# Optimization experiments

Hardware: AMD Instinct MI355X
Metric: run time of the kernel (lower is better)

Reference implementation:

```python
import jax, jax.numpy as jnp
import numpy as np

B, L, E, A, H = 1024, 200, 128, 128, 4

def setup_inputs() -> dict:
    key = jax.random.key(0)
    k1, k2, k3, k4, k5, k6 = jax.random.split(key, 6)
    inp = jax.random.normal(k1, (B, L, E), dtype=jnp.float32)
    mask = jax.random.randint(k2, (B, L), 0, 2).astype(bool)
    # guarantee at least one valid position per row (realistic: histories are non-empty)
    mask = mask.at[:, 0].set(True)
    pos_enc = jax.random.normal(k3, (1, L, E), dtype=jnp.float32)
    W1 = jax.random.normal(k4, (E, A), dtype=jnp.float32) / np.sqrt(E)
    W2 = jax.random.normal(k5, (A, H), dtype=jnp.float32) / np.sqrt(A)
    W_out = jax.random.normal(k6, (H * E, E), dtype=jnp.float32) / np.sqrt(H * E)
    return {"input": inp, "mask": mask, "pos_enc": pos_enc, "W1": W1, "W2": W2, "W_out": W_out}

def reference(input, mask, pos_enc, W1, W2, W_out):
    fm = mask.astype(input.dtype)[..., None]          # [B, L, 1]
    x = input * fm                                     # zero out padded positions
    xp = x + pos_enc                                   # broadcast [1, L, E]
    hidden = jnp.tanh(xp @ W1)                         # [B, L, A]
    att = hidden @ W2                                  # [B, L, H]
    att = jnp.swapaxes(att, 1, 2)                      # [B, H, L]
    neg = jnp.asarray(-(2.0 ** 32) + 1.0, dtype=att.dtype)
    att = jnp.where(mask[:, None, :], att, neg)
    att = jax.nn.softmax(att, axis=-1)                 # [B, H, L]
    pooled = jnp.einsum('bhl,ble->bhe', att, x)        # [B, H, E]
    flat = pooled.reshape(pooled.shape[0], -1)         # [B, H*E]
    return flat @ W_out                                # [B, E]
```

## Files before the change

kernel.cpp:

```cpp
#include <hip/hip_runtime.h>
#include <cfloat>

#define Bn 1024
#define Ln 200
#define En 128
#define An 128
#define Hn 4

#define WS_POSW1   0
#define WS_W1FRAG  106496
#define WS_ATTPOOL 139264
#define SLOT       1664
#define WS_WOUTT   1843200
#define WS_NEEDED  1974272

using f32x4  = __attribute__((ext_vector_type(4))) float;
using bf16x8 = __attribute__((ext_vector_type(8))) short;

__device__ __forceinline__ unsigned short f2bf(float f){
    unsigned u = __builtin_bit_cast(unsigned, f);
    u = (u + 0x7FFFu + ((u >> 16) & 1u)) >> 16;
    return (unsigned short)u;
}
__device__ __forceinline__ float bf2f(unsigned short s){
    unsigned u = ((unsigned)s) << 16;
    return __builtin_bit_cast(float, u);
}
__device__ __forceinline__ unsigned short f2h(float f){
    _Float16 h = (_Float16)f;
    return __builtin_bit_cast(unsigned short, h);
}
__device__ __forceinline__ float h2f(unsigned short s){
    _Float16 h = __builtin_bit_cast(_Float16, s);
    return (float)h;
}
__device__ __forceinline__ float tanh_cheap(float x){
    float e = __expf(2.f * x);
    float r = __builtin_amdgcn_rcpf(e + 1.f);
    return fmaf(-2.f, r, 1.f);
}
__device__ __forceinline__ float tanh_fast(float x){
    x = fminf(fmaxf(x, -12.f), 12.f);
    float e = __expf(2.f * x);
    return 1.f - 2.f / (e + 1.f);
}
__device__ __forceinline__ unsigned cvt_pk_bf16(float lo, float hi){
    unsigned r;
    asm("v_cvt_pk_bf16_f32 %0, %1, %2" : "=v"(r) : "v"(lo), "v"(hi));
    return r;
}
__device__ __forceinline__ int swz(int row, int k){
    return row * 128 + ((((k >> 3) ^ (row & 15)) << 3) | (k & 7));
}

__global__ __launch_bounds__(256) void sap_prep(
    const float* __restrict__ pos, const float* __restrict__ W1,
    const float* __restrict__ Wout, void* __restrict__ ws)
{
    const int t = threadIdx.x, blk = blockIdx.x;
    if (blk < 104){
        float* posW1 = (float*)((char*)ws + WS_POSW1);
        int l = blk * 2 + (t >> 7), a = t & 127;
        float acc = 0.f;
        if (l < Ln){
            #pragma unroll 4
            for (int k = 0; k < 128; ++k)
                acc += pos[l * En + k] * W1[k * An + a];
        }
        posW1[l * An + a] = acc;
    } else if (blk < 106){
        unsigned short* w1f = (unsigned short*)((char*)ws + WS_W1FRAG);
        int s = (blk - 104) * 256 + t;
        int lane = s & 63, A = s >> 6;
        int c = lane & 15, q = lane >> 4;
        #pragma unroll
        for (int ks = 0; ks < 4; ++ks){
            unsigned short v[8];
            #pragma unroll
            for (int j = 0; j < 8; ++j)
                v[j] = f2bf(W1[(ks * 32 + q * 8 + j) * An + A * 16 + c]);
            *(bf16x8*)&w1f[((s) * 4 + ks) * 8] = *(bf16x8*)v;
        }
    } else {
        unsigned short* wt = (unsigned short*)((char*)ws + WS_WOUTT);
        int flat = ((blk - 106) * 256 + t) * 4;
        int e = flat >> 9, k = flat & 511;
        unsigned short v[4];
        #pragma unroll
        for (int i = 0; i < 4; ++i)
            v[i] = f2bf(Wout[(size_t)(k + i) * En + e]);
        *(uint2*)&wt[flat] = *(uint2*)v;
    }
}

__global__ __launch_bounds__(512, 6) void sap_att5(
    const float* __restrict__ inp, const void* __restrict__ maskp,
    const float* __restrict__ W2, void* __restrict__ ws)
{
    __shared__ unsigned short s_x[64 * 128];
    __shared__ float s_part[8][4][64];
    __shared__ float s_mask[64];

    const int t = threadIdx.x, lane = t & 63, w = t >> 6;
    const int c = lane & 15, q = lane >> 4;
    const int b = blockIdx.x, chunk = blockIdx.y;
    const int l0 = chunk * 64;
    const int NT = (chunk < 3) ? 4 : 1;
    const int nv = (chunk < 3) ? 64 : (Ln - 192);

    const unsigned short* w1f   = (const unsigned short*)((char*)ws + WS_W1FRAG);
    const float*          posW1 = (const float*)((char*)ws + WS_POSW1);
    unsigned short*       slot  = (unsigned short*)((char*)ws + WS_ATTPOOL + (size_t)b * SLOT);

    {
        unsigned word = ((const unsigned*)maskp)[lane];
        unsigned long long bi = __ballot(word > 1u);
        unsigned long long bf = __ballot(word != 0u && word != 0x3F800000u);
        const int flag = (bi == 0ull) ? 0 : ((bf == 0ull) ? 2 : 1);
        if (t < 64){
            float m = 0.f;
            int l = l0 + t;
            if (l < Ln){
                int mv;
                if (flag == 0)      mv = ((const int*)maskp)[b * Ln + l] != 0;
                else if (flag == 1) mv = ((const unsigned char*)maskp)[b * Ln + l] != 0;
                else                mv = ((const float*)maskp)[b * Ln + l] != 0.f;
                m = mv ? 1.f : 0.f;
            }
            s_mask[t] = m;
        }
    }

    {
        const float4* in4 = (const float4*)(inp + ((size_t)b * Ln + l0) * En);
        if (chunk < 3){
            float4 u0 = in4[t], u1 = in4[t + 512], u2 = in4[t + 1024], u3 = in4[t + 1536];
            #define PUTV(vi, idx) { int ll = (idx) >> 5, kk = ((idx) & 31) * 4;               \
                uint2 val = make_uint2(cvt_pk_bf16(vi.x, vi.y), cvt_pk_bf16(vi.z, vi.w));     \
                *(uint2*)&s_x[swz(ll, kk)] = val; }
            PUTV(u0, t) PUTV(u1, t + 512) PUTV(u2, t + 1024) PUTV(u3, t + 1536)
            #undef PUTV
        } else {
            uint2 val = make_uint2(0u, 0u);
            if (t < 256){
                float4 u0 = in4[t];
                val = make_uint2(cvt_pk_bf16(u0.x, u0.y), cvt_pk_bf16(u0.z, u0.w));
            }
            int ll = t >> 5, kk = (t & 31) * 4;
            *(uint2*)&s_x[swz(ll, kk)] = val;
        }
    }

    bf16x8 af[4];
    #pragma unroll
    for (int ks = 0; ks < 4; ++ks)
        af[ks] = *(const bf16x8*)&w1f[((w * 64 + lane) * 4 + ks) * 8];
    float4 w2a[4];
    #pragma unroll
    for (int v = 0; v < 4; ++v)
        w2a[v] = *(const float4*)&W2[(w * 16 + q * 4 + v) * Hn];

    __syncthreads();

    for (int lt = 0; lt < NT; ++lt){
        int brow = lt * 16 + c;
        bf16x8 bfr[4];
        #pragma unroll
        for (int ks = 0; ks < 4; ++ks){
            int g = (ks * 4 + q) ^ c;
            bfr[ks] = *(bf16x8*)&s_x[brow * 128 + (g << 3)];
        }
        f32x4 acc = *(const f32x4*)&posW1[(size_t)(l0 + lt * 16 + c) * An + w * 16 + q * 4];
        #pragma unroll
        for (int ks = 0; ks < 4; ++ks)
            acc = __builtin_amdgcn_mfma_f32_16x16x32_bf16(af[ks], bfr[ks], acc, 0, 0, 0);
        float contrib[4] = {0.f, 0.f, 0.f, 0.f};
        #pragma unroll
        for (int v = 0; v < 4; ++v){
            float hv = tanh_cheap(acc[v]);
            contrib[0] += hv * w2a[v].x;
            contrib[1] += hv * w2a[v].y;
            contrib[2] += hv * w2a[v].z;
            contrib[3] += hv * w2a[v].w;
        }
        #pragma unroll
        for (int h = 0; h < 4; ++h){
            contrib[h] += __shfl_xor(contrib[h], 16, 64);
            contrib[h] += __shfl_xor(contrib[h], 32, 64);
        }
        s_part[w][q][lt * 16 + c] = contrib[q];
    }
    __syncthreads();

    if (t < 256){
        int h = t >> 6, ll = t & 63;
        if (ll < nv){
            float s = 0.f;
            #pragma unroll
            for (int w2 = 0; w2 < 8; ++w2) s += s_part[w2][h][ll];
            float v = (s_mask[ll] > 0.5f) ? s : -65504.f;
            slot[h * Ln + l0 + ll] = f2h(v);
        }
    }
}

__global__ __launch_bounds__(256, 8) void sap_pool(
    const float* __restrict__ inp, void* __restrict__ ws)
{
    __shared__ float s_att4[Ln * 4];
    __shared__ float s_scr[8][512];

    const int t = threadIdx.x, lane = t & 63, w = t >> 6;
    const int b = blockIdx.x;
    unsigned short* slot = (unsigned short*)((char*)ws + WS_ATTPOOL + (size_t)b * SLOT);

    {
        const int h = w;
        float v[4]; float mx = -FLT_MAX;
        #pragma unroll
        for (int i = 0; i < 4; ++i){
            int l = lane + i * 64;
            v[i] = (l < Ln) ? h2f(slot[h * Ln + l]) : -65504.f;
            mx = fmaxf(mx, v[i]);
        }
        for (int s = 32; s; s >>= 1) mx = fmaxf(mx, __shfl_xor(mx, s, 64));
        float e[4]; float sum = 0.f;
        #pragma unroll
        for (int i = 0; i < 4; ++i){
            int l = lane + i * 64;
            e[i] = (l < Ln) ? __expf(v[i] - mx) : 0.f;
            sum += e[i];
        }
        for (int s = 32; s; s >>= 1) sum += __shfl_xor(sum, s, 64);
        float inv = 1.f / sum;
        #pragma unroll
        for (int i = 0; i < 4; ++i){
            int l = lane + i * 64;
            if (l < Ln) s_att4[l * 4 + h] = e[i] * inv;
        }
    }
    __syncthreads();

    {
        const int eg = t & 31, r = t >> 5;
        const float* xin = inp + (size_t)b * (Ln * En);
        f32x4 acc0 = {0.f,0.f,0.f,0.f}, acc1 = acc0, acc2 = acc0, acc3 = acc0;
        for (int i = 0; i < 25; ++i){
            int l = i * 8 + r;
            f32x4 xv = *(const f32x4*)&xin[l * En + eg * 4];
            f32x4 a4 = *(const f32x4*)&s_att4[l * 4];
            acc0 += xv * a4[0];
            acc1 += xv * a4[1];
            acc2 += xv * a4[2];
            acc3 += xv * a4[3];
        }
        *(f32x4*)&s_scr[r][0 * 128 + eg * 4] = acc0;
        *(f32x4*)&s_scr[r][1 * 128 + eg * 4] = acc1;
        *(f32x4*)&s_scr[r][2 * 128 + eg * 4] = acc2;
        *(f32x4*)&s_scr[r][3 * 128 + eg * 4] = acc3;
    }
    __syncthreads();

    for (int s2 = t; s2 < 512; s2 += 256){
        float sum = 0.f;
        #pragma unroll
        for (int r2 = 0; r2 < 8; ++r2) sum += s_scr[r2][s2];
        slot[s2] = f2bf(sum);
    }
}

__global__ __launch_bounds__(256) void sap_out(
    const void* __restrict__ ws, float* __restrict__ out)
{
    const unsigned short* wt = (const unsigned short*)((const char*)ws + WS_WOUTT);
    const int t = threadIdx.x, lane = t & 63, w = t >> 6;
    const int c = lane & 15, q = lane >> 4;
    const int b0 = blockIdx.x * 16;
    const int e0 = (blockIdx.y * 4 + w) * 16;

    const unsigned short* pslot =
        (const unsigned short*)((const char*)ws + WS_ATTPOOL + (size_t)(b0 + c) * SLOT);

    f32x4 acc = {0.f, 0.f, 0.f, 0.f};
    #pragma unroll 4
    for (int ks = 0; ks < 16; ++ks){
        bf16x8 afr = *(const bf16x8*)&pslot[ks * 32 + q * 8];
        bf16x8 bfr = *(const bf16x8*)&wt[(e0 + c) * 512 + ks * 32 + q * 8];
        acc = __builtin_amdgcn_mfma_f32_16x16x32_bf16(afr, bfr, acc, 0, 0, 0);
    }
    #pragma unroll
    for (int v = 0; v < 4; ++v)
        out[(size_t)(b0 + q * 4 + v) * En + e0 + c] = acc[v];
}

__global__ __launch_bounds__(512, 4) void sap_fused_v2(
    const float* __restrict__ inp, const void* __restrict__ maskp,
    const float* __restrict__ pos, const float* __restrict__ W1,
    const float* __restrict__ W2, const float* __restrict__ Wout,
    float* __restrict__ out)
{
#define LP 208
    __shared__ unsigned short s_xp [LP * 128];
    __shared__ float s_att [4 * LP];
    __shared__ float s_mask[LP];
    __shared__ float s_pool[512];
    __shared__ float s_red [512];
    __shared__ int   s_flag;

    const int t = threadIdx.x;
    const int b = blockIdx.x;
    const int lane = t & 63, w = t >> 6;
    const int c = lane & 15, q = lane >> 4;

    if (t == 0){
        const unsigned* mw = (const unsigned*)maskp;
        int fi = 1, ff = 1;
        for (int i = 0; i < 64; ++i){
            unsigned word = mw[i];
            if (word > 1u) fi = 0;
            if (word != 0u && word != 0x3F800000u) ff = 0;
        }
        s_flag = fi ? 0 : (ff ? 2 : 1);
    }
    bf16x8 af[4];
    {
        const int arow = w * 16 + c;
        #pragma unroll
        for (int ks = 0; ks < 4; ++ks)
            #pragma unroll
            for (int j = 0; j < 8; ++j)
                af[ks][j] = (short)f2bf(W1[(ks * 32 + q * 8 + j) * An + arow]);
    }
    float w2a[4][4];
    #pragma unroll
    for (int v = 0; v < 4; ++v){
        float4 wv = *(const float4*)&W2[(w * 16 + q * 4 + v) * Hn];
        w2a[v][0] = wv.x; w2a[v][1] = wv.y; w2a[v][2] = wv.z; w2a[v][3] = wv.w;
    }
    __syncthreads();
    const int flag = s_flag;
    for (int l = t; l < LP; l += 512){
        float m = 0.f;
        if (l < Ln){
            int mv;
            if (flag == 0)      mv = ((const int*)maskp)[b * Ln + l] != 0;
            else if (flag == 1) mv = ((const unsigned char*)maskp)[b * Ln + l] != 0;
            else                mv = ((const float*)maskp)[b * Ln + l] != 0.f;
            m = mv ? 1.f : 0.f;
        }
        s_mask[l] = m;
    }
    for (int i = t; i < 4 * LP; i += 512) s_att[i] = 0.f;
    __syncthreads();
    {
        const float4* in4 = (const float4*)(inp + (size_t)b * (Ln * En));
        const float4* p4  = (const float4*)pos;
        #pragma unroll
        for (int it = 0; it < 13; ++it){
            int idx = it * 512 + t;
            int l = idx >> 5;
            int k = (idx & 31) * 4;
            uint2 val;
            if (idx < 6400){
                float m = s_mask[l];
                float4 a = in4[idx];
                float4 p = p4[idx];
                val = make_uint2((unsigned)f2bf(a.x*m+p.x) | ((unsigned)f2bf(a.y*m+p.y) << 16),
                                 (unsigned)f2bf(a.z*m+p.z) | ((unsigned)f2bf(a.w*m+p.w) << 16));
            } else val = make_uint2(0u, 0u);
            *(uint2*)&s_xp[swz(l, k)] = val;
        }
    }
    __syncthreads();
    for (int lt = 0; lt < 13; ++lt){
        int brow = lt * 16 + c;
        bf16x8 bfr[4];
        #pragma unroll
        for (int ks = 0; ks < 4; ++ks){
            int g = (ks * 4 + q) ^ c;
            bfr[ks] = *(bf16x8*)&s_xp[brow * 128 + (g << 3)];
        }
        f32x4 acc = {0.f, 0.f, 0.f, 0.f};
        #pragma unroll
        for (int ks = 0; ks < 4; ++ks)
            acc = __builtin_amdgcn_mfma_f32_16x16x32_bf16(af[ks], bfr[ks], acc, 0, 0, 0);
        float hv[4];
        #pragma unroll
        for (int v = 0; v < 4; ++v) hv[v] = tanh_fast(acc[v]);
        #pragma unroll
        for (int h = 0; h < 4; ++h){
            float contrib = hv[0]*w2a[0][h] + hv[1]*w2a[1][h] + hv[2]*w2a[2][h] + hv[3]*w2a[3][h];
            contrib += __shfl_xor(contrib, 16, 64);
            contrib += __shfl_xor(contrib, 32, 64);
            if (lane < 16) atomicAdd(&s_att[h * LP + lt * 16 + lane], contrib);
        }
    }
    __syncthreads();
    if (t < 256){
        const int sl = t & 63, h = t >> 6;
        float v[4]; bool ok[4]; float mx = -FLT_MAX;
        #pragma unroll
        for (int i = 0; i < 4; ++i){
            int l = sl + i * 64;
            ok[i] = (l < Ln) && (s_mask[l] > 0.5f);
            v[i]  = ok[i] ? s_att[h * LP + l] : -FLT_MAX;
            mx = fmaxf(mx, v[i]);
        }
        for (int s = 32; s; s >>= 1) mx = fmaxf(mx, __shfl_xor(mx, s, 64));
        float e[4]; float sum = 0.f;
        #pragma unroll
        for (int i = 0; i < 4; ++i){ e[i] = ok[i] ? __expf(v[i]-mx) : 0.f; sum += e[i]; }
        for (int s = 32; s; s >>= 1) sum += __shfl_xor(sum, s, 64);
        float inv = 1.f / sum;
        #pragma unroll
        for (int i = 0; i < 4; ++i){ int l = sl + i*64; if (l < LP) s_att[h*LP+l] = e[i]*inv; }
    }
    __syncthreads();
    {
        int h = t >> 7, e = t & 127;
        float acc = 0.f;
        #pragma unroll 4
        for (int l = 0; l < Ln; ++l){
            float xv = bf2f(s_xp[swz(l, e)]) - pos[l * En + e];
            acc += s_att[h * LP + l] * xv;
        }
        s_pool[h * En + e] = acc;
    }
    __syncthreads();
    {
        int qt = t >> 7, e = t & 127;
        float acc = 0.f;
        const float* wo = Wout + (size_t)(qt * 128) * En + e;
        #pragma unroll 4
        for (int i = 0; i < 128; ++i)
            acc += s_pool[qt * 128 + i] * wo[(size_t)i * En];
        s_red[t] = acc;
    }
    __syncthreads();
    if (t < 128)
        out[(size_t)b * En + t] = s_red[t] + s_red[t + 128] + s_red[t + 256] + s_red[t + 384];
#undef LP
}

extern "C" void kernel_launch(void* const* d_in, const int* in_sizes, int n_in,
                              void* d_out, int out_size, void* d_ws, size_t ws_size,
                              hipStream_t stream)
{
    const float* inp  = (const float*)d_in[0];
    const void*  mask = d_in[1];
    const float* pos  = (const float*)d_in[2];
    const float* W1   = (const float*)d_in[3];
    const float* W2   = (const float*)d_in[4];
    const float* Wout = (const float*)d_in[5];
    float* out = (float*)d_out;

    if (ws_size >= WS_NEEDED){
        sap_prep<<<170, 256, 0, stream>>>(pos, W1, Wout, d_ws);
        sap_att5<<<dim3(Bn, 4), 512, 0, stream>>>(inp, mask, W2, d_ws);
        sap_pool<<<Bn, 256, 0, stream>>>(inp, d_ws);
        sap_out<<<dim3(64, 2), 256, 0, stream>>>(d_ws, out);
    } else {
        sap_fused_v2<<<Bn, 512, 0, stream>>>(inp, mask, pos, W1, W2, Wout, out);
    }
}
```

Measured before the change: 70.63 us.

## Fuse attention scoring and pooling into one kernel with online softmax

Merges the per-chunk attention-score kernel and the softmax/pooling kernel into a single per-batch kernel. It walks the 200 positions in four 64-row chunks with a double-buffered bf16 LDS tile and keeps a running max and sum for softmax. Pooling reads the bf16 tile already staged in LDS, so the second global read of the input is gone, along with the fp16 score round-trip through the workspace and one launch. In exchange each block now has 4x less grid parallelism, runs serial chunk loops with extra barriers, and pools from bf16-rounded inputs instead of fp32.

Result: slower. 95.37 us (+35.0%).

```diff
diff --git a/kernel.cpp b/kernel.cpp
--- a/kernel.cpp
+++ b/kernel.cpp
@@ -25,14 +25,6 @@
 __device__ __forceinline__ float bf2f(unsigned short s){
     unsigned u = ((unsigned)s) << 16;
     return __builtin_bit_cast(float, u);
-}
-__device__ __forceinline__ unsigned short f2h(float f){
-    _Float16 h = (_Float16)f;
-    return __builtin_bit_cast(unsigned short, h);
-}
-__device__ __forceinline__ float h2f(unsigned short s){
-    _Float16 h = __builtin_bit_cast(_Float16, s);
-    return (float)h;
 }
 __device__ __forceinline__ float tanh_cheap(float x){
     float e = __expf(2.f * x);
@@ -71,7 +63,8 @@
     } else if (blk < 106){
         unsigned short* w1f = (unsigned short*)((char*)ws + WS_W1FRAG);
         int s = (blk - 104) * 256 + t;
-        int lane = s & 63, A = s >> 6;
+        int lane = s & 63;
+        int A = s >> 6;
         int c = lane & 15, q = lane >> 4;
         #pragma unroll
         for (int ks = 0; ks < 4; ++ks){
@@ -79,7 +72,7 @@
             #pragma unroll
             for (int j = 0; j < 8; ++j)
                 v[j] = f2bf(W1[(ks * 32 + q * 8 + j) * An + A * 16 + c]);
-            *(bf16x8*)&w1f[((s) * 4 + ks) * 8] = *(bf16x8*)v;
+            *(bf16x8*)&w1f[(s * 4 + ks) * 8] = *(bf16x8*)v;
         }
     } else {
         unsigned short* wt = (unsigned short*)((char*)ws + WS_WOUTT);
@@ -93,63 +86,24 @@
     }
 }
 
-__global__ __launch_bounds__(512, 6) void sap_att5(
+__global__ __launch_bounds__(512, 6) void sap_main3(
     const float* __restrict__ inp, const void* __restrict__ maskp,
     const float* __restrict__ W2, void* __restrict__ ws)
 {
-    __shared__ unsigned short s_x[64 * 128];
+    __shared__ unsigned short s_x[2][64 * 128];
     __shared__ float s_part[8][4][64];
-    __shared__ float s_mask[64];
+    __shared__ float s_w[4][64];
+    __shared__ float s_scale[4];
+    __shared__ float s_zfin[4];
 
     const int t = threadIdx.x, lane = t & 63, w = t >> 6;
     const int c = lane & 15, q = lane >> 4;
-    const int b = blockIdx.x, chunk = blockIdx.y;
-    const int l0 = chunk * 64;
-    const int NT = (chunk < 3) ? 4 : 1;
-    const int nv = (chunk < 3) ? 64 : (Ln - 192);
+    const int b = blockIdx.x;
+    const int hh = t >> 7, ee = t & 127;
 
     const unsigned short* w1f   = (const unsigned short*)((char*)ws + WS_W1FRAG);
     const float*          posW1 = (const float*)((char*)ws + WS_POSW1);
     unsigned short*       slot  = (unsigned short*)((char*)ws + WS_ATTPOOL + (size_t)b * SLOT);
-
-    {
-        unsigned word = ((const unsigned*)maskp)[lane];
-        unsigned long long bi = __ballot(word > 1u);
-        unsigned long long bf = __ballot(word != 0u && word != 0x3F800000u);
-        const int flag = (bi == 0ull) ? 0 : ((bf == 0ull) ? 2 : 1);
-        if (t < 64){
-            float m = 0.f;
-            int l = l0 + t;
-            if (l < Ln){
-                int mv;
-                if (flag == 0)      mv = ((const int*)maskp)[b * Ln + l] != 0;
-                else if (flag == 1) mv = ((const unsigned char*)maskp)[b * Ln + l] != 0;
-                else                mv = ((const float*)maskp)[b * Ln + l] != 0.f;
-                m = mv ? 1.f : 0.f;
-            }
-            s_mask[t] = m;
-        }
-    }
-
-    {
-        const float4* in4 = (const float4*)(inp + ((size_t)b * Ln + l0) * En);
-        if (chunk < 3){
-            float4 u0 = in4[t], u1 = in4[t + 512], u2 = in4[t + 1024], u3 = in4[t + 1536];
-            #define PUTV(vi, idx) { int ll = (idx) >> 5, kk = ((idx) & 31) * 4;               \
-                uint2 val = make_uint2(cvt_pk_bf16(vi.x, vi.y), cvt_pk_bf16(vi.z, vi.w));     \
-                *(uint2*)&s_x[swz(ll, kk)] = val; }
-            PUTV(u0, t) PUTV(u1, t + 512) PUTV(u2, t + 1024) PUTV(u3, t + 1536)
-            #undef PUTV
-        } else {
-            uint2 val = make_uint2(0u, 0u);
-            if (t < 256){
-                float4 u0 = in4[t];
-                val = make_uint2(cvt_pk_bf16(u0.x, u0.y), cvt_pk_bf16(u0.z, u0.w));
-            }
-            int ll = t >> 5, kk = (t & 31) * 4;
-            *(uint2*)&s_x[swz(ll, kk)] = val;
-        }
-    }
 
     bf16x8 af[4];
     #pragma unroll
@@ -160,113 +114,122 @@
     for (int v = 0; v < 4; ++v)
         w2a[v] = *(const float4*)&W2[(w * 16 + q * 4 + v) * Hn];
 
-    __syncthreads();
-
-    for (int lt = 0; lt < NT; ++lt){
-        int brow = lt * 16 + c;
-        bf16x8 bfr[4];
-        #pragma unroll
-        for (int ks = 0; ks < 4; ++ks){
-            int g = (ks * 4 + q) ^ c;
-            bfr[ks] = *(bf16x8*)&s_x[brow * 128 + (g << 3)];
-        }
-        f32x4 acc = *(const f32x4*)&posW1[(size_t)(l0 + lt * 16 + c) * An + w * 16 + q * 4];
-        #pragma unroll
-        for (int ks = 0; ks < 4; ++ks)
-            acc = __builtin_amdgcn_mfma_f32_16x16x32_bf16(af[ks], bfr[ks], acc, 0, 0, 0);
-        float contrib[4] = {0.f, 0.f, 0.f, 0.f};
-        #pragma unroll
-        for (int v = 0; v < 4; ++v){
-            float hv = tanh_cheap(acc[v]);
-            contrib[0] += hv * w2a[v].x;
-            contrib[1] += hv * w2a[v].y;
-            contrib[2] += hv * w2a[v].z;
-            contrib[3] += hv * w2a[v].w;
-        }
-        #pragma unroll
-        for (int h = 0; h < 4; ++h){
-            contrib[h] += __shfl_xor(contrib[h], 16, 64);
-            contrib[h] += __shfl_xor(contrib[h], 32, 64);
-        }
-        s_part[w][q][lt * 16 + c] = contrib[q];
-    }
-    __syncthreads();
-
-    if (t < 256){
-        int h = t >> 6, ll = t & 63;
-        if (ll < nv){
-            float s = 0.f;
-            #pragma unroll
-            for (int w2 = 0; w2 < 8; ++w2) s += s_part[w2][h][ll];
-            float v = (s_mask[ll] > 0.5f) ? s : -65504.f;
-            slot[h * Ln + l0 + ll] = f2h(v);
-        }
-    }
-}
-
-__global__ __launch_bounds__(256, 8) void sap_pool(
-    const float* __restrict__ inp, void* __restrict__ ws)
-{
-    __shared__ float s_att4[Ln * 4];
-    __shared__ float s_scr[8][512];
-
-    const int t = threadIdx.x, lane = t & 63, w = t >> 6;
-    const int b = blockIdx.x;
-    unsigned short* slot = (unsigned short*)((char*)ws + WS_ATTPOOL + (size_t)b * SLOT);
-
-    {
-        const int h = w;
-        float v[4]; float mx = -FLT_MAX;
-        #pragma unroll
-        for (int i = 0; i < 4; ++i){
-            int l = lane + i * 64;
-            v[i] = (l < Ln) ? h2f(slot[h * Ln + l]) : -65504.f;
-            mx = fmaxf(mx, v[i]);
-        }
-        for (int s = 32; s; s >>= 1) mx = fmaxf(mx, __shfl_xor(mx, s, 64));
-        float e[4]; float sum = 0.f;
-        #pragma unroll
-        for (int i = 0; i < 4; ++i){
-            int l = lane + i * 64;
-            e[i] = (l < Ln) ? __expf(v[i] - mx) : 0.f;
-            sum += e[i];
-        }
-        for (int s = 32; s; s >>= 1) sum += __shfl_xor(sum, s, 64);
-        float inv = 1.f / sum;
-        #pragma unroll
-        for (int i = 0; i < 4; ++i){
-            int l = lane + i * 64;
-            if (l < Ln) s_att4[l * 4 + h] = e[i] * inv;
-        }
-    }
-    __syncthreads();
-
-    {
-        const int eg = t & 31, r = t >> 5;
-        const float* xin = inp + (size_t)b * (Ln * En);
-        f32x4 acc0 = {0.f,0.f,0.f,0.f}, acc1 = acc0, acc2 = acc0, acc3 = acc0;
-        for (int i = 0; i < 25; ++i){
-            int l = i * 8 + r;
-            f32x4 xv = *(const f32x4*)&xin[l * En + eg * 4];
-            f32x4 a4 = *(const f32x4*)&s_att4[l * 4];
-            acc0 += xv * a4[0];
-            acc1 += xv * a4[1];
-            acc2 += xv * a4[2];
-            acc3 += xv * a4[3];
-        }
-        *(f32x4*)&s_scr[r][0 * 128 + eg * 4] = acc0;
-        *(f32x4*)&s_scr[r][1 * 128 + eg * 4] = acc1;
-        *(f32x4*)&s_scr[r][2 * 128 + eg * 4] = acc2;
-        *(f32x4*)&s_scr[r][3 * 128 + eg * 4] = acc3;
-    }
-    __syncthreads();
-
-    for (int s2 = t; s2 < 512; s2 += 256){
-        float sum = 0.f;
-        #pragma unroll
-        for (int r2 = 0; r2 < 8; ++r2) sum += s_scr[r2][s2];
-        slot[s2] = f2bf(sum);
-    }
+    int flag;
+    {
+        unsigned word = ((const unsigned*)maskp)[lane];
+        unsigned long long bi = __ballot(word > 1u);
+        unsigned long long bfm = __ballot(word != 0u && word != 0x3F800000u);
+        flag = (bi == 0ull) ? 0 : ((bfm == 0ull) ? 2 : 1);
+    }
+
+    const float4* in4 = (const float4*)(inp + (size_t)b * (Ln * En));
+
+    {
+        float4 u0 = in4[t], u1 = in4[t + 512], u2 = in4[t + 1024], u3 = in4[t + 1536];
+        #define PUTV(buf, vi, idx) { int ll = (idx) >> 5, kk = ((idx) & 31) * 4;             \
+            uint2 val = make_uint2(cvt_pk_bf16(vi.x, vi.y), cvt_pk_bf16(vi.z, vi.w));        \
+            *(uint2*)&s_x[buf][swz(ll, kk)] = val; }
+        PUTV(0, u0, t) PUTV(0, u1, t + 512) PUTV(0, u2, t + 1024) PUTV(0, u3, t + 1536)
+    }
+    __syncthreads();
+
+    float accp = 0.f;
+    float Mh = -3.0e38f, Zh = 0.f;
+
+    for (int cch = 0; cch < 4; ++cch){
+        const int cur = cch & 1;
+        const int NT = (cch < 3) ? 4 : 1;
+
+        for (int lt = 0; lt < NT; ++lt){
+            int brow = lt * 16 + c;
+            bf16x8 bfr[4];
+            #pragma unroll
+            for (int ks = 0; ks < 4; ++ks){
+                int g = (ks * 4 + q) ^ c;
+                bfr[ks] = *(bf16x8*)&s_x[cur][brow * 128 + (g << 3)];
+            }
+            f32x4 acc = *(const f32x4*)&posW1[(size_t)(cch * 64 + lt * 16 + c) * An + w * 16 + q * 4];
+            #pragma unroll
+            for (int ks = 0; ks < 4; ++ks)
+                acc = __builtin_amdgcn_mfma_f32_16x16x32_bf16(af[ks], bfr[ks], acc, 0, 0, 0);
+            float contrib[4] = {0.f, 0.f, 0.f, 0.f};
+            #pragma unroll
+            for (int v = 0; v < 4; ++v){
+                float hv = tanh_cheap(acc[v]);
+                contrib[0] += hv * w2a[v].x;
+                contrib[1] += hv * w2a[v].y;
+                contrib[2] += hv * w2a[v].z;
+                contrib[3] += hv * w2a[v].w;
+            }
+            #pragma unroll
+            for (int h = 0; h < 4; ++h){
+                contrib[h] += __shfl_xor(contrib[h], 16, 64);
+                contrib[h] += __shfl_xor(contrib[h], 32, 64);
+            }
+            s_part[w][q][lt * 16 + c] = contrib[q];
+        }
+        __syncthreads();
+
+        float4 u0, u1, u2, u3;
+        if (cch < 3){
+            const int base = (cch + 1) * 2048;
+            const float4 z4 = make_float4(0.f, 0.f, 0.f, 0.f);
+            u0 = (base + t        < 6400) ? in4[base + t]        : z4;
+            u1 = (base + t + 512  < 6400) ? in4[base + t + 512]  : z4;
+            u2 = (base + t + 1024 < 6400) ? in4[base + t + 1024] : z4;
+            u3 = (base + t + 1536 < 6400) ? in4[base + t + 1536] : z4;
+        }
+
+        if (t < 256){
+            const int h = t >> 6, l = t & 63;
+            float att = 0.f;
+            #pragma unroll
+            for (int w2 = 0; w2 < 8; ++w2) att += s_part[w2][h][l];
+            int gl = cch * 64 + l;
+            int mv = 0;
+            if (gl < Ln){
+                if (flag == 0)      mv = ((const int*)maskp)[b * Ln + gl] != 0;
+                else if (flag == 1) mv = ((const unsigned char*)maskp)[b * Ln + gl] != 0;
+                else                mv = ((const float*)maskp)[b * Ln + gl] != 0.f;
+            }
+            att = mv ? att : -1.0e30f;
+            float cm = att;
+            #pragma unroll
+            for (int s = 32; s; s >>= 1) cm = fmaxf(cm, __shfl_xor(cm, s, 64));
+            float Mn = fmaxf(Mh, cm);
+            float sc = __expf(Mh - Mn);
+            float wl = __expf(att - Mn);
+            float zc = wl;
+            #pragma unroll
+            for (int s = 32; s; s >>= 1) zc += __shfl_xor(zc, s, 64);
+            Zh = Zh * sc + zc;
+            Mh = Mn;
+            s_w[h][l] = wl;
+            if (l == 0){
+                s_scale[h] = sc;
+                if (cch == 3) s_zfin[h] = Zh;
+            }
+        }
+        __syncthreads();
+
+        {
+            float a = accp * s_scale[hh];
+            #pragma unroll 8
+            for (int l = 0; l < 64; ++l)
+                a = fmaf(s_w[hh][l], bf2f(s_x[cur][swz(l, ee)]), a);
+            accp = a;
+        }
+
+        if (cch < 3){
+            const int base = (cch + 1) * 2048, nxt = cur ^ 1;
+            (void)base;
+            PUTV(nxt, u0, t) PUTV(nxt, u1, t + 512) PUTV(nxt, u2, t + 1024) PUTV(nxt, u3, t + 1536)
+        }
+        __syncthreads();
+    }
+    #undef PUTV
+
+    slot[hh * En + ee] = f2bf(accp * (1.f / s_zfin[hh]));
 }
 
 __global__ __launch_bounds__(256) void sap_out(
@@ -456,8 +419,7 @@
 
     if (ws_size >= WS_NEEDED){
         sap_prep<<<170, 256, 0, stream>>>(pos, W1, Wout, d_ws);
-        sap_att5<<<dim3(Bn, 4), 512, 0, stream>>>(inp, mask, W2, d_ws);
-        sap_pool<<<Bn, 256, 0, stream>>>(inp, d_ws);
+        sap_main3<<<Bn, 512, 0, stream>>>(inp, mask, W2, d_ws);
         sap_out<<<dim3(64, 2), 256, 0, stream>>>(d_ws, out);
     } else {
         sap_fused_v2<<<Bn, 512, 0, stream>>>(inp, mask, pos, W1, W2, Wout, out);
```

## Fuse attention-score and pooling kernels into one per-batch block

Applied to the files above, without the earlier changes.

Merges the per-chunk attention-score kernel and the softmax/pooling kernel into a single kernel with one 512-thread block per batch row. The block loops over the four 64-position chunks, keeps the scores in shared memory in fp32, and then runs the softmax and weighted pooling in place. This removes one kernel launch and the fp16 score round trip through global workspace. In exchange the grid drops from 4096 to 1024 blocks, shared memory per block grows, and the chunk loop runs serially with two barriers per chunk, which may reduce parallelism and latency hiding.

Result: faster. 64.60 us (-8.5%).

```diff
diff --git a/kernel.cpp b/kernel.cpp
--- a/kernel.cpp
+++ b/kernel.cpp
@@ -25,14 +25,6 @@
 __device__ __forceinline__ float bf2f(unsigned short s){
     unsigned u = ((unsigned)s) << 16;
     return __builtin_bit_cast(float, u);
-}
-__device__ __forceinline__ unsigned short f2h(float f){
-    _Float16 h = (_Float16)f;
-    return __builtin_bit_cast(unsigned short, h);
-}
-__device__ __forceinline__ float h2f(unsigned short s){
-    _Float16 h = __builtin_bit_cast(_Float16, s);
-    return (float)h;
 }
 __device__ __forceinline__ float tanh_cheap(float x){
     float e = __expf(2.f * x);
@@ -71,7 +63,8 @@
     } else if (blk < 106){
         unsigned short* w1f = (unsigned short*)((char*)ws + WS_W1FRAG);
         int s = (blk - 104) * 256 + t;
-        int lane = s & 63, A = s >> 6;
+        int lane = s & 63;
+        int A = s >> 6;
         int c = lane & 15, q = lane >> 4;
         #pragma unroll
         for (int ks = 0; ks < 4; ++ks){
@@ -79,7 +72,7 @@
             #pragma unroll
             for (int j = 0; j < 8; ++j)
                 v[j] = f2bf(W1[(ks * 32 + q * 8 + j) * An + A * 16 + c]);
-            *(bf16x8*)&w1f[((s) * 4 + ks) * 8] = *(bf16x8*)v;
+            *(bf16x8*)&w1f[(s * 4 + ks) * 8] = *(bf16x8*)v;
         }
     } else {
         unsigned short* wt = (unsigned short*)((char*)ws + WS_WOUTT);
@@ -93,63 +86,23 @@
     }
 }
 
-__global__ __launch_bounds__(512, 6) void sap_att5(
+__global__ __launch_bounds__(512, 4) void sap_att7(
     const float* __restrict__ inp, const void* __restrict__ maskp,
     const float* __restrict__ W2, void* __restrict__ ws)
 {
     __shared__ unsigned short s_x[64 * 128];
     __shared__ float s_part[8][4][64];
-    __shared__ float s_mask[64];
+    __shared__ float s_att4[208 * 4];
+    __shared__ float s_scr[16][512];
+    __shared__ float s_mask[256];
 
     const int t = threadIdx.x, lane = t & 63, w = t >> 6;
     const int c = lane & 15, q = lane >> 4;
-    const int b = blockIdx.x, chunk = blockIdx.y;
-    const int l0 = chunk * 64;
-    const int NT = (chunk < 3) ? 4 : 1;
-    const int nv = (chunk < 3) ? 64 : (Ln - 192);
+    const int b = blockIdx.x;
 
     const unsigned short* w1f   = (const unsigned short*)((char*)ws + WS_W1FRAG);
     const float*          posW1 = (const float*)((char*)ws + WS_POSW1);
     unsigned short*       slot  = (unsigned short*)((char*)ws + WS_ATTPOOL + (size_t)b * SLOT);
-
-    {
-        unsigned word = ((const unsigned*)maskp)[lane];
-        unsigned long long bi = __ballot(word > 1u);
-        unsigned long long bf = __ballot(word != 0u && word != 0x3F800000u);
-        const int flag = (bi == 0ull) ? 0 : ((bf == 0ull) ? 2 : 1);
-        if (t < 64){
-            float m = 0.f;
-            int l = l0 + t;
-            if (l < Ln){
-                int mv;
-                if (flag == 0)      mv = ((const int*)maskp)[b * Ln + l] != 0;
-                else if (flag == 1) mv = ((const unsigned char*)maskp)[b * Ln + l] != 0;
-                else                mv = ((const float*)maskp)[b * Ln + l] != 0.f;
-                m = mv ? 1.f : 0.f;
-            }
-            s_mask[t] = m;
-        }
-    }
-
-    {
-        const float4* in4 = (const float4*)(inp + ((size_t)b * Ln + l0) * En);
-        if (chunk < 3){
-            float4 u0 = in4[t], u1 = in4[t + 512], u2 = in4[t + 1024], u3 = in4[t + 1536];
-            #define PUTV(vi, idx) { int ll = (idx) >> 5, kk = ((idx) & 31) * 4;               \
-                uint2 val = make_uint2(cvt_pk_bf16(vi.x, vi.y), cvt_pk_bf16(vi.z, vi.w));     \
-                *(uint2*)&s_x[swz(ll, kk)] = val; }
-            PUTV(u0, t) PUTV(u1, t + 512) PUTV(u2, t + 1024) PUTV(u3, t + 1536)
-            #undef PUTV
-        } else {
-            uint2 val = make_uint2(0u, 0u);
-            if (t < 256){
-                float4 u0 = in4[t];
-                val = make_uint2(cvt_pk_bf16(u0.x, u0.y), cvt_pk_bf16(u0.z, u0.w));
-            }
-            int ll = t >> 5, kk = (t & 31) * 4;
-            *(uint2*)&s_x[swz(ll, kk)] = val;
-        }
-    }
 
     bf16x8 af[4];
     #pragma unroll
@@ -160,74 +113,104 @@
     for (int v = 0; v < 4; ++v)
         w2a[v] = *(const float4*)&W2[(w * 16 + q * 4 + v) * Hn];
 
-    __syncthreads();
-
-    for (int lt = 0; lt < NT; ++lt){
-        int brow = lt * 16 + c;
-        bf16x8 bfr[4];
-        #pragma unroll
-        for (int ks = 0; ks < 4; ++ks){
-            int g = (ks * 4 + q) ^ c;
-            bfr[ks] = *(bf16x8*)&s_x[brow * 128 + (g << 3)];
-        }
-        f32x4 acc = *(const f32x4*)&posW1[(size_t)(l0 + lt * 16 + c) * An + w * 16 + q * 4];
-        #pragma unroll
-        for (int ks = 0; ks < 4; ++ks)
-            acc = __builtin_amdgcn_mfma_f32_16x16x32_bf16(af[ks], bfr[ks], acc, 0, 0, 0);
-        float contrib[4] = {0.f, 0.f, 0.f, 0.f};
-        #pragma unroll
-        for (int v = 0; v < 4; ++v){
-            float hv = tanh_cheap(acc[v]);
-            contrib[0] += hv * w2a[v].x;
-            contrib[1] += hv * w2a[v].y;
-            contrib[2] += hv * w2a[v].z;
-            contrib[3] += hv * w2a[v].w;
-        }
-        #pragma unroll
-        for (int h = 0; h < 4; ++h){
-            contrib[h] += __shfl_xor(contrib[h], 16, 64);
-            contrib[h] += __shfl_xor(contrib[h], 32, 64);
-        }
-        s_part[w][q][lt * 16 + c] = contrib[q];
+    {
+        unsigned word = ((const unsigned*)maskp)[lane];
+        unsigned long long bi  = __ballot(word > 1u);
+        unsigned long long bfm = __ballot(word != 0u && word != 0x3F800000u);
+        int flag = (bi == 0ull) ? 0 : ((bfm == 0ull) ? 2 : 1);
+        if (t < 256){
+            float m = 0.f;
+            if (t < Ln){
+                int mv;
+                if (flag == 0)      mv = ((const int*)maskp)[b * Ln + t] != 0;
+                else if (flag == 1) mv = ((const unsigned char*)maskp)[b * Ln + t] != 0;
+                else                mv = ((const float*)maskp)[b * Ln + t] != 0.f;
+                m = mv ? 1.f : 0.f;
+            }
+            s_mask[t] = m;
+        }
+    }
+
+    for (int cch = 0; cch < 4; ++cch){
+        const int NT = (cch < 3) ? 4 : 1;
+
+        {
+            const float4* in4 = (const float4*)(inp + (size_t)b * (Ln * En) + cch * 64 * En);
+            #define PUTV(vi, idx) { int ll = (idx) >> 5, kk = ((idx) & 31) * 4;            \
+                uint2 val = make_uint2(cvt_pk_bf16(vi.x, vi.y), cvt_pk_bf16(vi.z, vi.w));  \
+                *(uint2*)&s_x[swz(ll, kk)] = val; }
+            if (cch < 3){
+                float4 u0 = in4[t], u1 = in4[t + 512], u2 = in4[t + 1024], u3 = in4[t + 1536];
+                PUTV(u0, t) PUTV(u1, t + 512) PUTV(u2, t + 1024) PUTV(u3, t + 1536)
+            } else {
+                uint2 val = make_uint2(0u, 0u);
+                if (t < 256){
+                    float4 u0 = in4[t];
+                    val = make_uint2(cvt_pk_bf16(u0.x, u0.y), cvt_pk_bf16(u0.z, u0.w));
+                }
+                int ll = t >> 5, kk = (t & 31) * 4;
+                *(uint2*)&s_x[swz(ll, kk)] = val;
+            }
+            #undef PUTV
+        }
+        __syncthreads();
+
+        for (int lt = 0; lt < NT; ++lt){
+            int brow = lt * 16 + c;
+            bf16x8 bfr[4];
+            #pragma unroll
+            for (int ks = 0; ks < 4; ++ks){
+                int g = (ks * 4 + q) ^ c;
+                bfr[ks] = *(bf16x8*)&s_x[brow * 128 + (g << 3)];
+            }
+            f32x4 acc = *(const f32x4*)&posW1[(size_t)(cch * 64 + brow) * An + w * 16 + q * 4];
+            #pragma unroll
+            for (int ks = 0; ks < 4; ++ks)
+                acc = __builtin_amdgcn_mfma_f32_16x16x32_bf16(af[ks], bfr[ks], acc, 0, 0, 0);
+            float contrib[4] = {0.f, 0.f, 0.f, 0.f};
+            #pragma unroll
+            for (int v = 0; v < 4; ++v){
+                float hv = tanh_cheap(acc[v]);
+                contrib[0] += hv * w2a[v].x;
+                contrib[1] += hv * w2a[v].y;
+                contrib[2] += hv * w2a[v].z;
+                contrib[3] += hv * w2a[v].w;
+            }
+            #pragma unroll
+            for (int h = 0; h < 4; ++h){
+                contrib[h] += __shfl_xor(contrib[h], 16, 64);
+                contrib[h] += __shfl_xor(contrib[h], 32, 64);
+            }
+            s_part[w][q][lt * 16 + c] = contrib[q];
+        }
+        __syncthreads();
+
+        if (t < 256){
+            int h = t >> 6, l = t & 63, gl = cch * 64 + l;
+            if (gl < Ln){
+                float a = 0.f;
+                #pragma unroll
+                for (int w2 = 0; w2 < 8; ++w2) a += s_part[w2][h][l];
+                s_att4[gl * 4 + h] = (s_mask[gl] > 0.5f) ? a : -1.0e30f;
+            }
+        }
     }
     __syncthreads();
 
     if (t < 256){
-        int h = t >> 6, ll = t & 63;
-        if (ll < nv){
-            float s = 0.f;
-            #pragma unroll
-            for (int w2 = 0; w2 < 8; ++w2) s += s_part[w2][h][ll];
-            float v = (s_mask[ll] > 0.5f) ? s : -65504.f;
-            slot[h * Ln + l0 + ll] = f2h(v);
-        }
-    }
-}
-
-__global__ __launch_bounds__(256, 8) void sap_pool(
-    const float* __restrict__ inp, void* __restrict__ ws)
-{
-    __shared__ float s_att4[Ln * 4];
-    __shared__ float s_scr[8][512];
-
-    const int t = threadIdx.x, lane = t & 63, w = t >> 6;
-    const int b = blockIdx.x;
-    unsigned short* slot = (unsigned short*)((char*)ws + WS_ATTPOOL + (size_t)b * SLOT);
-
-    {
-        const int h = w;
+        const int h = t >> 6, sl = t & 63;
         float v[4]; float mx = -FLT_MAX;
         #pragma unroll
         for (int i = 0; i < 4; ++i){
-            int l = lane + i * 64;
-            v[i] = (l < Ln) ? h2f(slot[h * Ln + l]) : -65504.f;
+            int l = sl + i * 64;
+            v[i] = (l < Ln) ? s_att4[l * 4 + h] : -3.0e38f;
             mx = fmaxf(mx, v[i]);
         }
         for (int s = 32; s; s >>= 1) mx = fmaxf(mx, __shfl_xor(mx, s, 64));
         float e[4]; float sum = 0.f;
         #pragma unroll
         for (int i = 0; i < 4; ++i){
-            int l = lane + i * 64;
+            int l = sl + i * 64;
             e[i] = (l < Ln) ? __expf(v[i] - mx) : 0.f;
             sum += e[i];
         }
@@ -235,7 +218,7 @@
         float inv = 1.f / sum;
         #pragma unroll
         for (int i = 0; i < 4; ++i){
-            int l = lane + i * 64;
+            int l = sl + i * 64;
             if (l < Ln) s_att4[l * 4 + h] = e[i] * inv;
         }
     }
@@ -244,28 +227,30 @@
     {
         const int eg = t & 31, r = t >> 5;
         const float* xin = inp + (size_t)b * (Ln * En);
-        f32x4 acc0 = {0.f,0.f,0.f,0.f}, acc1 = acc0, acc2 = acc0, acc3 = acc0;
-        for (int i = 0; i < 25; ++i){
-            int l = i * 8 + r;
-            f32x4 xv = *(const f32x4*)&xin[l * En + eg * 4];
-            f32x4 a4 = *(const f32x4*)&s_att4[l * 4];
-            acc0 += xv * a4[0];
-            acc1 += xv * a4[1];
-            acc2 += xv * a4[2];
-            acc3 += xv * a4[3];
-        }
-        *(f32x4*)&s_scr[r][0 * 128 + eg * 4] = acc0;
-        *(f32x4*)&s_scr[r][1 * 128 + eg * 4] = acc1;
-        *(f32x4*)&s_scr[r][2 * 128 + eg * 4] = acc2;
-        *(f32x4*)&s_scr[r][3 * 128 + eg * 4] = acc3;
-    }
-    __syncthreads();
-
-    for (int s2 = t; s2 < 512; s2 += 256){
+        f32x4 a0 = {0.f,0.f,0.f,0.f}, a1 = a0, a2 = a0, a3 = a0;
+        for (int i = 0; i < 13; ++i){
+            int l = i * 16 + r;
+            if (l < Ln){
+                f32x4 xv = *(const f32x4*)&xin[l * En + eg * 4];
+                f32x4 w4 = *(const f32x4*)&s_att4[l * 4];
+                a0 += xv * w4[0];
+                a1 += xv * w4[1];
+                a2 += xv * w4[2];
+                a3 += xv * w4[3];
+            }
+        }
+        *(f32x4*)&s_scr[r][0 * 128 + eg * 4] = a0;
+        *(f32x4*)&s_scr[r][1 * 128 + eg * 4] = a1;
+        *(f32x4*)&s_scr[r][2 * 128 + eg * 4] = a2;
+        *(f32x4*)&s_scr[r][3 * 128 + eg * 4] = a3;
+    }
+    __syncthreads();
+
+    {
         float sum = 0.f;
         #pragma unroll
-        for (int r2 = 0; r2 < 8; ++r2) sum += s_scr[r2][s2];
-        slot[s2] = f2bf(sum);
+        for (int r2 = 0; r2 < 16; ++r2) sum += s_scr[r2][t];
+        slot[t] = f2bf(sum);
     }
 }
 
@@ -456,8 +441,7 @@
 
     if (ws_size >= WS_NEEDED){
         sap_prep<<<170, 256, 0, stream>>>(pos, W1, Wout, d_ws);
-        sap_att5<<<dim3(Bn, 4), 512, 0, stream>>>(inp, mask, W2, d_ws);
-        sap_pool<<<Bn, 256, 0, stream>>>(inp, d_ws);
+        sap_att7<<<Bn, 512, 0, stream>>>(inp, mask, W2, d_ws);
         sap_out<<<dim3(64, 2), 256, 0, stream>>>(d_ws, out);
     } else {
         sap_fused_v2<<<Bn, 512, 0, stream>>>(inp, mask, pos, W1, W2, Wout, out);
```
